# Kernel tuning notes

Hardware: AMD Instinct MI355X
Metric: run time of the kernel (lower is better)

## Reference

```python
import jax, jax.numpy as jnp
import numpy as np

NUM_HEADS = 8
N_CHUNKS = 4


def _chunk_bounds(n, chunks):
    # replicate torch.chunk: chunk size = ceil(n/chunks), last chunk smaller
    cs = -(-n // chunks)
    return [min(i * cs, n) for i in range(chunks + 1)]


def setup_inputs() -> dict:
    key = jax.random.key(0)
    ks = jax.random.split(key, 9)
    dim, N, B = 512, 289, 256
    C = dim // 2
    H, d = NUM_HEADS, C // NUM_HEADS
    return {
        "x1": jax.random.normal(ks[0], (B, N, dim), jnp.float32),
        "x2": jax.random.normal(ks[1], (B, N, dim), jnp.float32),
        "W_reduce": jax.random.normal(ks[2], (dim, C), jnp.float32) * 0.02,
        "W_qkv": jax.random.normal(ks[3], (C, 3 * C), jnp.float32) * 0.02,
        "W_proj": jax.random.normal(ks[4], (C, dim), jnp.float32) * 0.02,
        "b_proj": jnp.zeros((dim,), jnp.float32),
        "w_ds": 1.0 + 0.02 * jax.random.normal(ks[5], (H, d), jnp.float32),
        "w_uds": 1.0 + 0.02 * jax.random.normal(ks[6], (H, d), jnp.float32),
        "b_uds": jnp.zeros((H, d), jnp.float32),
    }


def _branch(x, W_reduce, W_qkv, W_proj, b_proj, w_ds, w_uds, b_uds, use_ds):
    xr = x @ W_reduce                       # [B, N, C]
    B, N, C = xr.shape
    H = NUM_HEADS
    d = C // H
    scale = d ** -0.5
    qkv = (xr @ W_qkv).reshape(B, N, 3, H, d).transpose(2, 0, 3, 1, 4)  # [3,B,H,N,d]
    q, k, v = qkv[0], qkv[1], qkv[2]
    bounds = _chunk_bounds(N, N_CHUNKS)
    outs = []
    for i in range(N_CHUNKS):               # fixed 4-way chunking, per original
        s, e = bounds[i], bounds[i + 1]
        qc, kc, vc = q[:, :, s:e], k[:, :, s:e], v[:, :, s:e]
        if use_ds:
            # Distributive: learned per-head diagonal metric on head_dim, scale folded in
            attn = jnp.einsum('bhnd,bhmd->bhnm', qc * w_ds[None, :, None, :], kc) * scale
        else:
            # UnDistributive: learned per-head affine on q and k, then scaled dot-product
            qc = qc * w_uds[None, :, None, :] + b_uds[None, :, None, :]
            kc = kc * w_uds[None, :, None, :] + b_uds[None, :, None, :]
            attn = jnp.einsum('bhnd,bhmd->bhnm', qc, kc) * scale
        attn = jax.nn.softmax(attn, axis=-1)
        outs.append(jnp.einsum('bhnm,bhmd->bnhd', attn, vc))  # (attn @ v).transpose(1,2)
    o = jnp.concatenate(outs, axis=1).reshape(B, N, C)
    return o @ W_proj + b_proj


def reference(x1, x2, W_reduce, W_qkv, W_proj, b_proj, w_ds, w_uds, b_uds):
    y1 = _branch(x1, W_reduce, W_qkv, W_proj, b_proj, w_ds, w_uds, b_uds, use_ds=True)
    y2 = _branch(x2, W_reduce, W_qkv, W_proj, b_proj, w_ds, w_uds, b_uds, use_ds=False)
    return (y1, y2)
```

## Files before the change

kernel.cpp:

```cpp
#include <hip/hip_runtime.h>

typedef __bf16 bf16;
typedef bf16 bf16x4 __attribute__((ext_vector_type(4)));
typedef bf16 bf16x8 __attribute__((ext_vector_type(8)));
typedef float f32x4 __attribute__((ext_vector_type(4)));

#define LOG2E 1.4426950408889634f

__device__ __forceinline__ f32x4 mfma16(bf16x8 a, bf16x8 b, f32x4 c) {
    return __builtin_amdgcn_mfma_f32_16x16x32_bf16(a, b, c, 0, 0, 0);
}

__device__ __forceinline__ void async16(const void* g, void* l) {
    __builtin_amdgcn_global_load_lds(
        (const __attribute__((address_space(1))) void*)g,
        (__attribute__((address_space(3))) void*)l, 16, 0, 0);
}

__global__ __launch_bounds__(256) void prep_w(
    const float* __restrict__ Wr, const float* __restrict__ Wq,
    const float* __restrict__ w_ds, const float* __restrict__ w_uds,
    const float* __restrict__ b_uds,
    bf16* __restrict__ W1t, bf16* __restrict__ W2t, float* __restrict__ bias) {
    __shared__ float wq[256][17];
    const int t = threadIdx.x;
    const int k0 = blockIdx.x * 64, n0 = blockIdx.y * 16, z = blockIdx.z;
#pragma unroll
    for (int i = 0; i < 16; i++) {
        int c = i * 16 + (t >> 4);
        wq[c][t & 15] = Wq[c * 768 + n0 + (t & 15)];
    }
    __syncthreads();
    const int j = t & 15, n = n0 + j;
    const float rs = 0.17677669529663687f;
    float scale, bv;
    if (z == 0) {
        scale = (n < 256) ? w_ds[n] * rs : 1.f; bv = 0.f;
    } else if (n < 256) {
        scale = w_uds[n] * rs; bv = b_uds[n] * rs;
    } else if (n < 512) {
        scale = w_uds[n - 256]; bv = b_uds[n - 256];
    } else {
        scale = 1.f; bv = 0.f;
    }
    bf16* Wt = z ? W2t : W1t;
#pragma unroll 1
    for (int i = 0; i < 4; i++) {
        int k = k0 + (t >> 4) * 4 + i;
        float acc = 0.f;
        for (int c = 0; c < 256; c++) acc = fmaf(Wr[k * 256 + c], wq[c][j], acc);
        Wt[n * 512 + k] = (bf16)(acc * scale);
    }
    if (blockIdx.x == 0 && (t >> 4) == 0) bias[z * 768 + n] = bv;
}

__global__ void prep_wp(const float* __restrict__ Wp, bf16* __restrict__ Wpt) {
    const int n = blockIdx.x, k = threadIdx.x;
    Wpt[n * 256 + k] = (bf16)Wp[k * 512 + n];
}

__global__ __launch_bounds__(256) void xcast(const float* __restrict__ X1,
                                             const float* __restrict__ X2,
                                             bf16* __restrict__ O1,
                                             bf16* __restrict__ O2) {
    const float* X = blockIdx.y ? X2 : X1;
    bf16* O = blockIdx.y ? O2 : O1;
    const long total = 37879808;
    const long stride = (long)gridDim.x * 256 * 8;
    for (long i = ((long)blockIdx.x * 256 + threadIdx.x) * 8; i < total; i += stride) {
        float4 a = *(const float4*)&X[i];
        float4 b = *(const float4*)&X[i + 4];
        bf16x8 w = {(bf16)a.x, (bf16)a.y, (bf16)a.z, (bf16)a.w,
                    (bf16)b.x, (bf16)b.y, (bf16)b.z, (bf16)b.w};
        *(bf16x8*)&O[i] = w;
    }
}

template <int KT, int KS, int LDO, int OUTF32>
__device__ __forceinline__ void gemm8(const bf16* __restrict__ A,
                                      const bf16* __restrict__ B,
                                      const float* __restrict__ biasp,
                                      void* __restrict__ OutP, bf16* Lf) {
    const int tid = threadIdx.x;
    const int lane = tid & 63, wave = tid >> 6;
    const int ln = lane & 15, quad = lane >> 4;
    const int wm = wave >> 2, wn = wave & 3;
    const int bn = blockIdx.x * 256, bm = blockIdx.y * 256;
    f32x4 acc[8][4] = {};
    float bi[4];
#pragma unroll
    for (int nr = 0; nr < 4; nr++) bi[nr] = biasp[bn + wn * 64 + nr * 16 + ln];

    const int srow = tid >> 2;
    const int schunk = ((tid & 3) ^ ((tid >> 3) & 3)) * 8;
    const int rq = (quad ^ ((ln >> 1) & 3)) * 8;
    const int abase = (wm * 128 + ln) * 32 + rq;
    const int bbase = 16384 + (wn * 64 + ln) * 32 + rq;

    auto stA = [&](int buf, int kk, int h, int kb) {
        async16(&A[(long)(bm + h * 128 + srow) * KS + kb + kk * 32 + schunk],
                Lf + buf * 32768 + kk * 8192 + (h * 128 + wave * 16) * 32);
    };
    auto stB = [&](int buf, int kk, int h, int kb) {
        async16(&B[(long)(bn + h * 128 + srow) * KS + kb + kk * 32 + schunk],
                Lf + buf * 32768 + 16384 + kk * 8192 + (h * 128 + wave * 16) * 32);
    };

    stA(0, 0, 0, 0); stA(0, 0, 1, 0); stB(0, 0, 0, 0); stB(0, 0, 1, 0);
    stA(0, 1, 0, 0); stA(0, 1, 1, 0); stB(0, 1, 0, 0); stB(0, 1, 1, 0);

#pragma unroll 1
    for (int kt = 0; kt < KT; ++kt) {
        const int cb = kt & 1, nb = cb ^ 1, kb = (kt + 1) * 64;
        const bool pf = (kt + 1) < KT;
        const int aoff = cb * 32768 + abase;
        const int boff = cb * 32768 + bbase;
        bf16x8 aF[4], bF[4], aG[4];
        asm volatile("s_waitcnt vmcnt(4)" ::: "memory");
        __builtin_amdgcn_s_barrier();
        asm volatile("" ::: "memory");
#pragma unroll
        for (int i = 0; i < 4; i++) aF[i] = *(const bf16x8*)&Lf[aoff + i * 512];
#pragma unroll
        for (int i = 0; i < 4; i++) bF[i] = *(const bf16x8*)&Lf[boff + i * 512];
        if (pf) { stA(nb, 0, 0, kb); stA(nb, 0, 1, kb); }
        __builtin_amdgcn_s_setprio(1);
#pragma unroll
        for (int i = 0; i < 4; i++)
#pragma unroll
            for (int j = 0; j < 4; j++) acc[i][j] = mfma16(aF[i], bF[j], acc[i][j]);
        __builtin_amdgcn_s_setprio(0);
        asm volatile("" ::: "memory");
        __builtin_amdgcn_s_barrier();
        asm volatile("" ::: "memory");
#pragma unroll
        for (int i = 0; i < 4; i++) aG[i] = *(const bf16x8*)&Lf[aoff + (i + 4) * 512];
        if (pf) { stB(nb, 0, 0, kb); stB(nb, 0, 1, kb); }
        __builtin_amdgcn_s_setprio(1);
#pragma unroll
        for (int i = 0; i < 4; i++)
#pragma unroll
            for (int j = 0; j < 4; j++) acc[i + 4][j] = mfma16(aG[i], bF[j], acc[i + 4][j]);
        __builtin_amdgcn_s_setprio(0);
        if (pf) asm volatile("s_waitcnt vmcnt(4)" ::: "memory");
        else    asm volatile("s_waitcnt vmcnt(0)" ::: "memory");
        __builtin_amdgcn_s_barrier();
        asm volatile("" ::: "memory");
#pragma unroll
        for (int i = 0; i < 4; i++) aF[i] = *(const bf16x8*)&Lf[aoff + 8192 + i * 512];
#pragma unroll
        for (int i = 0; i < 4; i++) bF[i] = *(const bf16x8*)&Lf[boff + 8192 + i * 512];
        if (pf) { stA(nb, 1, 0, kb); stA(nb, 1, 1, kb); }
        __builtin_amdgcn_s_setprio(1);
#pragma unroll
        for (int i = 0; i < 4; i++)
#pragma unroll
            for (int j = 0; j < 4; j++) acc[i][j] = mfma16(aF[i], bF[j], acc[i][j]);
        __builtin_amdgcn_s_setprio(0);
        asm volatile("" ::: "memory");
        __builtin_amdgcn_s_barrier();
        asm volatile("" ::: "memory");
#pragma unroll
        for (int i = 0; i < 4; i++) aG[i] = *(const bf16x8*)&Lf[aoff + 8192 + (i + 4) * 512];
        if (pf) { stB(nb, 1, 0, kb); stB(nb, 1, 1, kb); }
        __builtin_amdgcn_s_setprio(1);
#pragma unroll
        for (int i = 0; i < 4; i++)
#pragma unroll
            for (int j = 0; j < 4; j++) acc[i + 4][j] = mfma16(aG[i], bF[j], acc[i + 4][j]);
        __builtin_amdgcn_s_setprio(0);
    }
#pragma unroll
    for (int i = 0; i < 8; i++)
#pragma unroll
        for (int j = 0; j < 4; j++) {
            const int col = bn + wn * 64 + j * 16 + ln;
            const long row0 = bm + wm * 128 + i * 16 + quad * 4;
            if (OUTF32) {
                float* Y = (float*)OutP;
#pragma unroll
                for (int r = 0; r < 4; r++)
                    Y[(row0 + r) * LDO + col] = acc[i][j][r] + bi[j];
            } else {
                bf16* Y = (bf16*)OutP;
#pragma unroll
                for (int r = 0; r < 4; r++)
                    Y[(row0 + r) * LDO + col] = (bf16)(acc[i][j][r] + bi[j]);
            }
        }
}

__global__ __launch_bounds__(512, 2) void gemm_qkv8(
    const bf16* __restrict__ X, const bf16* __restrict__ Wt,
    const float* __restrict__ biasp, bf16* __restrict__ Out) {
    __shared__ __attribute__((aligned(16))) bf16 L[65536];
    gemm8<8, 512, 768, 0>(X, Wt, biasp, Out, L);
}

__global__ __launch_bounds__(512, 2) void gemm_proj8(
    const bf16* __restrict__ Ain, const bf16* __restrict__ Wpt,
    const float* __restrict__ bp, float* __restrict__ Y) {
    __shared__ __attribute__((aligned(16))) bf16 L[65536];
    gemm8<4, 256, 512, 1>(Ain, Wpt, bp, Y, L);
}

__global__ __launch_bounds__(256) void attn(const bf16* __restrict__ QKV,
                                            bf16* __restrict__ O) {
    __shared__ __attribute__((aligned(16))) bf16 vT[4][32 * 104];
    __shared__ __attribute__((aligned(16))) bf16 P[4][16 * 104];
    const int tid = threadIdx.x;
    const int lane = tid & 63, wave = tid >> 6;
    const int ln = lane & 15, quad = lane >> 4;
    const int chunk = blockIdx.x, b = blockIdx.y;
    const int s = chunk * 73;
    const int mc = min(289 - s, 73);
    const int rowbase = b * 289 + s;
    bf16* vTw = &vT[wave][0];
    bf16* Pw = &P[wave][0];
    const f32x4 zero4 = {0.f, 0.f, 0.f, 0.f};

    {
        bf16x4 z = {(bf16)0.f, (bf16)0.f, (bf16)0.f, (bf16)0.f};
        *(bf16x4*)&Pw[(lane >> 2) * 104 + 80 + (lane & 3) * 4] = z;
    }

#pragma unroll 1
    for (int hi = 0; hi < 2; hi++) {
        const int h = wave + hi * 4;
        const int cq = h * 32, ck = 256 + h * 32, cv = 512 + h * 32;

#pragma unroll
        for (int p5 = 0; p5 < 6; p5++) {
            int m = p5 * 16 + (lane >> 2);
            int mr = min(m, mc - 1);
            bf16x8 v8 = *(const bf16x8*)&QKV[(rowbase + mr) * 768 + cv + (lane & 3) * 8];
            int d0 = (lane & 3) * 8;
#pragma unroll
            for (int j = 0; j < 8; j++) vTw[(d0 + j) * 104 + m] = v8[j];
        }
        bf16x8 kf[5];
#pragma unroll
        for (int mt = 0; mt < 5; mt++) {
            int mr = min(mt * 16 + ln, mc - 1);
            kf[mt] = *(const bf16x8*)&QKV[(rowbase + mr) * 768 + ck + quad * 8];
        }
        bf16x8 vf[2][3];
#pragma unroll
        for (int dt = 0; dt < 2; dt++)
#pragma unroll
            for (int mk = 0; mk < 3; mk++)
                vf[dt][mk] = *(const bf16x8*)&vTw[(dt * 16 + ln) * 104 + mk * 32 + quad * 8];

#pragma unroll 1
        for (int nt = 0; nt < 5; nt++) {
            int qr = min(nt * 16 + ln, mc - 1);
            bf16x8 qf = *(const bf16x8*)&QKV[(rowbase + qr) * 768 + cq + quad * 8];
            f32x4 S[5];
#pragma unroll
            for (int mt = 0; mt < 5; mt++) S[mt] = mfma16(qf, kf[mt], zero4);
#pragma unroll
            for (int mt = 0; mt < 5; mt++)
                if (mt * 16 + ln >= mc) {
                    S[mt][0] = -1e30f; S[mt][1] = -1e30f;
                    S[mt][2] = -1e30f; S[mt][3] = -1e30f;
                }
            float mxv[4], sm[4];
#pragma unroll
            for (int r = 0; r < 4; r++) {
                float m0 = S[0][r];
#pragma unroll
                for (int mt = 1; mt < 5; mt++) m0 = fmaxf(m0, S[mt][r]);
                m0 = fmaxf(m0, __shfl_xor(m0, 1));
                m0 = fmaxf(m0, __shfl_xor(m0, 2));
                m0 = fmaxf(m0, __shfl_xor(m0, 4));
                m0 = fmaxf(m0, __shfl_xor(m0, 8));
                mxv[r] = m0;
                sm[r] = 0.f;
            }
#pragma unroll
            for (int mt = 0; mt < 5; mt++)
#pragma unroll
                for (int r = 0; r < 4; r++) {
                    float p = exp2f((S[mt][r] - mxv[r]) * LOG2E);
                    sm[r] += p;
                    Pw[(quad * 4 + r) * 104 + mt * 16 + ln] = (bf16)p;
                }
#pragma unroll
            for (int r = 0; r < 4; r++) {
                float t = sm[r];
                t += __shfl_xor(t, 1);
                t += __shfl_xor(t, 2);
                t += __shfl_xor(t, 4);
                t += __shfl_xor(t, 8);
                sm[r] = 1.0f / t;
            }
            f32x4 o0 = zero4, o1 = zero4;
#pragma unroll
            for (int mk = 0; mk < 3; mk++) {
                bf16x8 pa = *(const bf16x8*)&Pw[ln * 104 + mk * 32 + quad * 8];
                o0 = mfma16(pa, vf[0][mk], o0);
                o1 = mfma16(pa, vf[1][mk], o1);
            }
#pragma unroll
            for (int r = 0; r < 4; r++) {
                int nl = nt * 16 + quad * 4 + r;
                if (nl < mc) {
                    int orow = (rowbase + nl) * 256 + h * 32;
                    O[orow + ln] = (bf16)(o0[r] * sm[r]);
                    O[orow + 16 + ln] = (bf16)(o1[r] * sm[r]);
                }
            }
        }
    }
}

extern "C" void kernel_launch(void* const* d_in, const int* in_sizes, int n_in,
                              void* d_out, int out_size, void* d_ws, size_t ws_size,
                              hipStream_t stream) {
    (void)in_sizes; (void)n_in; (void)out_size; (void)ws_size;
    const float* x1 = (const float*)d_in[0];
    const float* x2 = (const float*)d_in[1];
    const float* Wr = (const float*)d_in[2];
    const float* Wq = (const float*)d_in[3];
    const float* Wp = (const float*)d_in[4];
    const float* bp = (const float*)d_in[5];
    const float* w_ds = (const float*)d_in[6];
    const float* w_uds = (const float*)d_in[7];
    const float* b_uds = (const float*)d_in[8];

    char* ws = (char*)d_ws;
    bf16* W1t = (bf16*)(ws);
    bf16* W2t = (bf16*)(ws + 786432);
    bf16* Wpt = (bf16*)(ws + 1572864);
    float* bias = (float*)(ws + 1835008);
    bf16* ob = (bf16*)(ws + 1841152);
    float* out = (float*)d_out;
    char* outc = (char*)d_out;
    bf16* Xb1 = (bf16*)(outc);
    bf16* Xb2 = (bf16*)(outc + 75759616);
    bf16* qkv = (bf16*)(outc + 151519232);

    prep_w<<<dim3(8, 48, 2), 256, 0, stream>>>(Wr, Wq, w_ds, w_uds, b_uds, W1t, W2t, bias);
    prep_wp<<<dim3(512), 256, 0, stream>>>(Wp, Wpt);
    xcast<<<dim3(2048, 2), 256, 0, stream>>>(x1, x2, Xb1, Xb2);

    gemm_qkv8<<<dim3(3, 289), 512, 0, stream>>>(Xb1, W1t, bias, qkv);
    attn<<<dim3(4, 256), 256, 0, stream>>>(qkv, ob);
    gemm_qkv8<<<dim3(3, 289), 512, 0, stream>>>(Xb2, W2t, bias + 768, qkv);
    gemm_proj8<<<dim3(2, 289), 512, 0, stream>>>(ob, Wpt, bp, out);
    attn<<<dim3(4, 256), 256, 0, stream>>>(qkv, ob);
    gemm_proj8<<<dim3(2, 289), 512, 0, stream>>>(ob, Wpt, bp, out + (size_t)37879808);
}
```

Before: 897.0 us.

## Fuse prep kernels and batch both branches into single launches via grid z

Merges the three preprocessing kernels into one launch that splits its block index range by role. When the workspace is large enough, it moves the bf16 inputs and QKV buffers into workspace and runs both branches' QKV GEMM, attention and projection GEMM as single launches with blockIdx.z selecting the branch. This cuts the launch count and gives each launch twice the blocks, which should fill the GPU better. The cost is a larger workspace footprint, and the old serial path is kept as a fallback.

```diff
diff --git a/kernel.cpp b/kernel.cpp
--- a/kernel.cpp
+++ b/kernel.cpp
@@ -17,62 +17,63 @@
         (__attribute__((address_space(3))) void*)l, 16, 0, 0);
 }
 
-__global__ __launch_bounds__(256) void prep_w(
+__global__ __launch_bounds__(256) void megaprep(
     const float* __restrict__ Wr, const float* __restrict__ Wq,
     const float* __restrict__ w_ds, const float* __restrict__ w_uds,
-    const float* __restrict__ b_uds,
-    bf16* __restrict__ W1t, bf16* __restrict__ W2t, float* __restrict__ bias) {
+    const float* __restrict__ b_uds, const float* __restrict__ Wp,
+    const float* __restrict__ x1, const float* __restrict__ x2,
+    bf16* __restrict__ W1t, bf16* __restrict__ W2t, bf16* __restrict__ Wpt,
+    float* __restrict__ bias, bf16* __restrict__ Xb1, bf16* __restrict__ Xb2) {
     __shared__ float wq[256][17];
+    const int id = blockIdx.x;
     const int t = threadIdx.x;
-    const int k0 = blockIdx.x * 64, n0 = blockIdx.y * 16, z = blockIdx.z;
-#pragma unroll
-    for (int i = 0; i < 16; i++) {
-        int c = i * 16 + (t >> 4);
-        wq[c][t & 15] = Wq[c * 768 + n0 + (t & 15)];
-    }
-    __syncthreads();
-    const int j = t & 15, n = n0 + j;
-    const float rs = 0.17677669529663687f;
-    float scale, bv;
-    if (z == 0) {
-        scale = (n < 256) ? w_ds[n] * rs : 1.f; bv = 0.f;
-    } else if (n < 256) {
-        scale = w_uds[n] * rs; bv = b_uds[n] * rs;
-    } else if (n < 512) {
-        scale = w_uds[n - 256]; bv = b_uds[n - 256];
+    if (id < 768) {
+        const int kx = id & 7, ny = (id >> 3) % 48, z = id / 384;
+        const int k0 = kx * 64, n0 = ny * 16;
+#pragma unroll
+        for (int i = 0; i < 16; i++) {
+            int c = i * 16 + (t >> 4);
+            wq[c][t & 15] = Wq[c * 768 + n0 + (t & 15)];
+        }
+        __syncthreads();
+        const int j = t & 15, n = n0 + j;
+        const float rs = 0.17677669529663687f;
+        float scale, bv;
+        if (z == 0) {
+            scale = (n < 256) ? w_ds[n] * rs : 1.f; bv = 0.f;
+        } else if (n < 256) {
+            scale = w_uds[n] * rs; bv = b_uds[n] * rs;
+        } else if (n < 512) {
+            scale = w_uds[n - 256]; bv = b_uds[n - 256];
+        } else {
+            scale = 1.f; bv = 0.f;
+        }
+        bf16* Wt = z ? W2t : W1t;
+#pragma unroll 1
+        for (int i = 0; i < 4; i++) {
+            int k = k0 + (t >> 4) * 4 + i;
+            float acc = 0.f;
+            for (int c = 0; c < 256; c++) acc = fmaf(Wr[k * 256 + c], wq[c][j], acc);
+            Wt[n * 512 + k] = (bf16)(acc * scale);
+        }
+        if (kx == 0 && (t >> 4) == 0) bias[z * 768 + n] = bv;
+    } else if (id < 1280) {
+        const int n = id - 768, k = t;
+        Wpt[n * 256 + k] = (bf16)Wp[k * 512 + n];
     } else {
-        scale = 1.f; bv = 0.f;
-    }
-    bf16* Wt = z ? W2t : W1t;
-#pragma unroll 1
-    for (int i = 0; i < 4; i++) {
-        int k = k0 + (t >> 4) * 4 + i;
-        float acc = 0.f;
-        for (int c = 0; c < 256; c++) acc = fmaf(Wr[k * 256 + c], wq[c][j], acc);
-        Wt[n * 512 + k] = (bf16)(acc * scale);
-    }
-    if (blockIdx.x == 0 && (t >> 4) == 0) bias[z * 768 + n] = bv;
-}
-
-__global__ void prep_wp(const float* __restrict__ Wp, bf16* __restrict__ Wpt) {
-    const int n = blockIdx.x, k = threadIdx.x;
-    Wpt[n * 256 + k] = (bf16)Wp[k * 512 + n];
-}
-
-__global__ __launch_bounds__(256) void xcast(const float* __restrict__ X1,
-                                             const float* __restrict__ X2,
-                                             bf16* __restrict__ O1,
-                                             bf16* __restrict__ O2) {
-    const float* X = blockIdx.y ? X2 : X1;
-    bf16* O = blockIdx.y ? O2 : O1;
-    const long total = 37879808;
-    const long stride = (long)gridDim.x * 256 * 8;
-    for (long i = ((long)blockIdx.x * 256 + threadIdx.x) * 8; i < total; i += stride) {
-        float4 a = *(const float4*)&X[i];
-        float4 b = *(const float4*)&X[i + 4];
-        bf16x8 w = {(bf16)a.x, (bf16)a.y, (bf16)a.z, (bf16)a.w,
-                    (bf16)b.x, (bf16)b.y, (bf16)b.z, (bf16)b.w};
-        *(bf16x8*)&O[i] = w;
+        const int i0 = id - 1280;
+        const int by = i0 >> 11, bx = i0 & 2047;
+        const float* X = by ? x2 : x1;
+        bf16* O = by ? Xb2 : Xb1;
+        const long total = 37879808;
+        const long stride = (long)2048 * 256 * 8;
+        for (long i = ((long)bx * 256 + t) * 8; i < total; i += stride) {
+            float4 a = *(const float4*)&X[i];
+            float4 b = *(const float4*)&X[i + 4];
+            bf16x8 w = {(bf16)a.x, (bf16)a.y, (bf16)a.z, (bf16)a.w,
+                        (bf16)b.x, (bf16)b.y, (bf16)b.z, (bf16)b.w};
+            *(bf16x8*)&O[i] = w;
+        }
     }
 }
 
@@ -191,23 +192,34 @@
 }
 
 __global__ __launch_bounds__(512, 2) void gemm_qkv8(
-    const bf16* __restrict__ X, const bf16* __restrict__ Wt,
-    const float* __restrict__ biasp, bf16* __restrict__ Out) {
+    const bf16* __restrict__ X1, const bf16* __restrict__ X2,
+    const bf16* __restrict__ W1t, const bf16* __restrict__ W2t,
+    const float* __restrict__ biasp, bf16* __restrict__ O1,
+    bf16* __restrict__ O2) {
     __shared__ __attribute__((aligned(16))) bf16 L[65536];
-    gemm8<8, 512, 768, 0>(X, Wt, biasp, Out, L);
+    const int z = blockIdx.z;
+    gemm8<8, 512, 768, 0>(z ? X2 : X1, z ? W2t : W1t, biasp + z * 768,
+                          z ? O2 : O1, L);
 }
 
 __global__ __launch_bounds__(512, 2) void gemm_proj8(
-    const bf16* __restrict__ Ain, const bf16* __restrict__ Wpt,
-    const float* __restrict__ bp, float* __restrict__ Y) {
+    const bf16* __restrict__ A1, const bf16* __restrict__ A2,
+    const bf16* __restrict__ Wpt, const float* __restrict__ bp,
+    float* __restrict__ Y) {
     __shared__ __attribute__((aligned(16))) bf16 L[65536];
-    gemm8<4, 256, 512, 1>(Ain, Wpt, bp, Y, L);
-}
-
-__global__ __launch_bounds__(256) void attn(const bf16* __restrict__ QKV,
-                                            bf16* __restrict__ O) {
+    const int z = blockIdx.z;
+    gemm8<4, 256, 512, 1>(z ? A2 : A1, Wpt, bp, Y + (size_t)z * 37879808, L);
+}
+
+__global__ __launch_bounds__(256) void attn(const bf16* __restrict__ QKV1,
+                                            const bf16* __restrict__ QKV2,
+                                            bf16* __restrict__ O1,
+                                            bf16* __restrict__ O2) {
     __shared__ __attribute__((aligned(16))) bf16 vT[4][32 * 104];
     __shared__ __attribute__((aligned(16))) bf16 P[4][16 * 104];
+    const int z = blockIdx.z;
+    const bf16* QKV = z ? QKV2 : QKV1;
+    bf16* O = z ? O2 : O1;
     const int tid = threadIdx.x;
     const int lane = tid & 63, wave = tid >> 6;
     const int ln = lane & 15, quad = lane >> 4;
@@ -220,8 +232,8 @@
     const f32x4 zero4 = {0.f, 0.f, 0.f, 0.f};
 
     {
-        bf16x4 z = {(bf16)0.f, (bf16)0.f, (bf16)0.f, (bf16)0.f};
-        *(bf16x4*)&Pw[(lane >> 2) * 104 + 80 + (lane & 3) * 4] = z;
+        bf16x4 zz = {(bf16)0.f, (bf16)0.f, (bf16)0.f, (bf16)0.f};
+        *(bf16x4*)&Pw[(lane >> 2) * 104 + 80 + (lane & 3) * 4] = zz;
     }
 
 #pragma unroll 1
@@ -317,7 +329,7 @@
 extern "C" void kernel_launch(void* const* d_in, const int* in_sizes, int n_in,
                               void* d_out, int out_size, void* d_ws, size_t ws_size,
                               hipStream_t stream) {
-    (void)in_sizes; (void)n_in; (void)out_size; (void)ws_size;
+    (void)in_sizes; (void)n_in; (void)out_size;
     const float* x1 = (const float*)d_in[0];
     const float* x2 = (const float*)d_in[1];
     const float* Wr = (const float*)d_in[2];
@@ -333,21 +345,38 @@
     bf16* W2t = (bf16*)(ws + 786432);
     bf16* Wpt = (bf16*)(ws + 1572864);
     float* bias = (float*)(ws + 1835008);
-    bf16* ob = (bf16*)(ws + 1841152);
+    bf16* ob1 = (bf16*)(ws + 1841152);
     float* out = (float*)d_out;
     char* outc = (char*)d_out;
-    bf16* Xb1 = (bf16*)(outc);
-    bf16* Xb2 = (bf16*)(outc + 75759616);
-    bf16* qkv = (bf16*)(outc + 151519232);
-
-    prep_w<<<dim3(8, 48, 2), 256, 0, stream>>>(Wr, Wq, w_ds, w_uds, b_uds, W1t, W2t, bias);
-    prep_wp<<<dim3(512), 256, 0, stream>>>(Wp, Wpt);
-    xcast<<<dim3(2048, 2), 256, 0, stream>>>(x1, x2, Xb1, Xb2);
-
-    gemm_qkv8<<<dim3(3, 289), 512, 0, stream>>>(Xb1, W1t, bias, qkv);
-    attn<<<dim3(4, 256), 256, 0, stream>>>(qkv, ob);
-    gemm_qkv8<<<dim3(3, 289), 512, 0, stream>>>(Xb2, W2t, bias + 768, qkv);
-    gemm_proj8<<<dim3(2, 289), 512, 0, stream>>>(ob, Wpt, bp, out);
-    attn<<<dim3(4, 256), 256, 0, stream>>>(qkv, ob);
-    gemm_proj8<<<dim3(2, 289), 512, 0, stream>>>(ob, Wpt, bp, out + (size_t)37879808);
-}
+
+    if (ws_size >= (size_t)456398848) {
+        bf16* Xb1 = (bf16*)(ws + 39720960);
+        bf16* Xb2 = (bf16*)(ws + 115480576);
+        bf16* qkv1 = (bf16*)(ws + 191240192);
+        bf16* qkv2 = (bf16*)(ws + 304879616);
+        bf16* ob2 = (bf16*)(ws + 418519040);
+        megaprep<<<dim3(5376), 256, 0, stream>>>(Wr, Wq, w_ds, w_uds, b_uds, Wp,
+                                                 x1, x2, W1t, W2t, Wpt, bias,
+                                                 Xb1, Xb2);
+        gemm_qkv8<<<dim3(3, 289, 2), 512, 0, stream>>>(Xb1, Xb2, W1t, W2t, bias,
+                                                       qkv1, qkv2);
+        attn<<<dim3(4, 256, 2), 256, 0, stream>>>(qkv1, qkv2, ob1, ob2);
+        gemm_proj8<<<dim3(2, 289, 2), 512, 0, stream>>>(ob1, ob2, Wpt, bp, out);
+    } else {
+        bf16* Xb1 = (bf16*)(outc);
+        bf16* Xb2 = (bf16*)(outc + 75759616);
+        bf16* qkv = (bf16*)(outc + 151519232);
+        megaprep<<<dim3(5376), 256, 0, stream>>>(Wr, Wq, w_ds, w_uds, b_uds, Wp,
+                                                 x1, x2, W1t, W2t, Wpt, bias,
+                                                 Xb1, Xb2);
+        gemm_qkv8<<<dim3(3, 289, 1), 512, 0, stream>>>(Xb1, Xb1, W1t, W1t, bias,
+                                                       qkv, qkv);
+        attn<<<dim3(4, 256, 1), 256, 0, stream>>>(qkv, qkv, ob1, ob1);
+        gemm_qkv8<<<dim3(3, 289, 1), 512, 0, stream>>>(Xb2, Xb2, W2t, W2t,
+                                                       bias + 768, qkv, qkv);
+        gemm_proj8<<<dim3(2, 289, 1), 512, 0, stream>>>(ob1, ob1, Wpt, bp, out);
+        attn<<<dim3(4, 256, 1), 256, 0, stream>>>(qkv, qkv, ob1, ob1);
+        gemm_proj8<<<dim3(2, 289, 1), 512, 0, stream>>>(ob1, ob1, Wpt, bp,
+                                                        out + (size_t)37879808);
+    }
+}
```

Measured after the change: 846.7 us. -5.6%, faster.
